# Performance work log

Measured on AMD Instinct MI355X. Metric: run time of the kernel, lower is better.

## Reference

```python
import jax, jax.numpy as jnp
import numpy as np

NUM_GROUPS = 32
EPS = 1e-6


def group_norm(x, gamma, beta):
    # x: [B, C, H, W]
    b, c, h, w = x.shape
    xg = x.reshape(b, NUM_GROUPS, c // NUM_GROUPS, h, w)
    mean = xg.mean(axis=(2, 3, 4), keepdims=True)
    var = xg.var(axis=(2, 3, 4), keepdims=True)
    xn = ((xg - mean) * jax.lax.rsqrt(var + EPS)).reshape(b, c, h, w)
    return xn * gamma[None, :, None, None] + beta[None, :, None, None]


def setup_inputs() -> dict:
    key = jax.random.key(0)
    ks = jax.random.split(key, 10)
    B, C, H, W = 2, 512, 64, 64
    s = 1.0 / np.sqrt(C)
    return {
        "x": jax.random.normal(ks[0], (B, C, H, W), dtype=jnp.float32),
        "gamma": jnp.ones((C,), jnp.float32),
        "beta": jnp.zeros((C,), jnp.float32),
        "Wq": jax.random.normal(ks[1], (C, C), jnp.float32) * s,
        "bq": jnp.zeros((C,), jnp.float32),
        "Wk": jax.random.normal(ks[2], (C, C), jnp.float32) * s,
        "bk": jnp.zeros((C,), jnp.float32),
        "Wv": jax.random.normal(ks[3], (C, C), jnp.float32) * s,
        "bv": jnp.zeros((C,), jnp.float32),
        "Wo": jax.random.normal(ks[4], (C, C), jnp.float32) * s,
        "bo": jnp.zeros((C,), jnp.float32),
    }


def reference(x, gamma, beta, Wq, bq, Wk, bk, Wv, bv, Wo, bo):
    b, c, h, w = x.shape
    hn = group_norm(x, gamma, beta)               # [B,C,H,W]
    hf = hn.reshape(b, c, h * w)                  # [B,C,N]
    # 1x1 convs == channel matmuls
    q = jnp.einsum('oc,bcn->bon', Wq, hf) + bq[None, :, None]
    k = jnp.einsum('oc,bcn->bon', Wk, hf) + bk[None, :, None]
    v = jnp.einsum('oc,bcn->bon', Wv, hf) + bv[None, :, None]
    scale = float(c) ** -0.5
    scores = jnp.einsum('bci,bcj->bij', q, k) * scale   # [B,N,N]
    attn = jax.nn.softmax(scores, axis=-1)
    out = jnp.einsum('bij,bcj->bci', attn, v)            # [B,C,N]
    out = jnp.einsum('oc,bcn->bon', Wo, out) + bo[None, :, None]
    return x + out.reshape(b, c, h, w)
```

## Files before the change

kernel.cpp:

```cpp
#include <hip/hip_runtime.h>

#define BB 2
#define CC 512
#define NS 4096
#define NGROUP 32
#define TILE 128
#define RSTRIDE 132

typedef __bf16 bf16_8 __attribute__((ext_vector_type(8)));
typedef __bf16 bf16_4 __attribute__((ext_vector_type(4)));
typedef float f32_4 __attribute__((ext_vector_type(4)));

#define SMEM_BYTES 33792

__device__ __forceinline__ void gld_lds16(const __bf16* g, __bf16* l) {
  __builtin_amdgcn_global_load_lds(
      (const __attribute__((address_space(1))) unsigned int*)g,
      (__attribute__((address_space(3))) unsigned int*)l, 16, 0, 0);
}

__global__ __launch_bounds__(256) void gn_stats(const float* __restrict__ x,
                                                float* __restrict__ stats) {
  const float4* p = (const float4*)(x + (size_t)blockIdx.x * 65536);
  float s = 0.f, q = 0.f;
  for (int i = threadIdx.x; i < 16384; i += 256) {
    float4 v = p[i];
    s += v.x + v.y + v.z + v.w;
    q += v.x * v.x + v.y * v.y + v.z * v.z + v.w * v.w;
  }
#pragma unroll
  for (int off = 32; off > 0; off >>= 1) {
    s += __shfl_down(s, off, 64);
    q += __shfl_down(q, off, 64);
  }
  __shared__ float ls[4], lq[4];
  int wave = threadIdx.x >> 6, lane = threadIdx.x & 63;
  if (lane == 0) { ls[wave] = s; lq[wave] = q; }
  __syncthreads();
  if (threadIdx.x == 0) {
    float S = ls[0] + ls[1] + ls[2] + ls[3];
    float Q = lq[0] + lq[1] + lq[2] + lq[3];
    float mean = S * (1.f / 65536.f);
    float var = Q * (1.f / 65536.f) - mean * mean;
    stats[blockIdx.x * 2] = mean;
    stats[blockIdx.x * 2 + 1] = rsqrtf(var + 1e-6f);
  }
}

__global__ __launch_bounds__(256) void gn_apply_t(const float* __restrict__ x,
                                                  const float* __restrict__ stats,
                                                  const float* __restrict__ gamma,
                                                  const float* __restrict__ beta,
                                                  __bf16* __restrict__ hnT) {
  __shared__ float tile[32][33];
  int b = blockIdx.z;
  int c0 = blockIdx.y * 32;
  int n0 = blockIdx.x * 32;
  int tx = threadIdx.x;
  int ty = threadIdx.y;
  const float* xb = x + (size_t)b * CC * NS;
#pragma unroll
  for (int i = 0; i < 4; i++) {
    int c = c0 + ty + i * 8;
    float mean = stats[(b * NGROUP + (c >> 4)) * 2 + 0];
    float rstd = stats[(b * NGROUP + (c >> 4)) * 2 + 1];
    float v = xb[(size_t)c * NS + n0 + tx];
    tile[ty + i * 8][tx] = (v - mean) * rstd * gamma[c] + beta[c];
  }
  __syncthreads();
  __bf16* out = hnT + (size_t)b * NS * CC;
#pragma unroll
  for (int i = 0; i < 4; i++) {
    int n = n0 + ty + i * 8;
    out[(size_t)n * CC + c0 + tx] = (__bf16)tile[tx][ty + i * 8];
  }
}

__global__ __launch_bounds__(256) void cvt_w(const float* __restrict__ w0, const float* __restrict__ w1,
                                             const float* __restrict__ w2, const float* __restrict__ w3,
                                             __bf16* __restrict__ o0, __bf16* __restrict__ o1,
                                             __bf16* __restrict__ o2, __bf16* __restrict__ o3) {
  int tsel = blockIdx.x >> 8;
  int i = (blockIdx.x & 255) * 256 + threadIdx.x;
  const float* src = tsel == 0 ? w0 : tsel == 1 ? w1 : tsel == 2 ? w2 : w3;
  __bf16* dst = tsel == 0 ? o0 : tsel == 1 ? o1 : tsel == 2 ? o2 : o3;
  float4 v = ((const float4*)src)[i];
  bf16_4 r;
  r[0] = (__bf16)v.x; r[1] = (__bf16)v.y; r[2] = (__bf16)v.z; r[3] = (__bf16)v.w;
  ((bf16_4*)dst)[i] = r;
}

__device__ __forceinline__ void gemm_core(const __bf16* __restrict__ A, const __bf16* __restrict__ B,
                                          int K, int lda, int ldb,
                                          __bf16* lA, __bf16* lB, f32_4 (&acc)[4][2]) {
  const int t = threadIdx.x;
  const int lane = t & 63;
  const int wave = t >> 6;
  const int lrow = lane & 15, quad = lane >> 4;
  const int wrow = (wave >> 2) * 64, wcol = (wave & 3) * 32;
  const int co = (quad ^ ((lrow >> 1) & 3)) * 8;
  const int r0 = t >> 2;
  const int kp = ((t & 3) ^ ((t >> 3) & 3)) * 8;
  const __bf16* pA = A + (size_t)r0 * lda + kp;
  const __bf16* pB = B + (size_t)r0 * ldb + kp;
  for (int k0 = 0; k0 < K; k0 += 64) {
    __syncthreads();
    gld_lds16(pA + k0,      &lA[t * 8]);
    gld_lds16(pA + k0 + 32, &lA[4096 + t * 8]);
    gld_lds16(pB + k0,      &lB[t * 8]);
    gld_lds16(pB + k0 + 32, &lB[4096 + t * 8]);
    __syncthreads();
#pragma unroll
    for (int ks = 0; ks < 2; ks++) {
      const __bf16* la = lA + ks * 4096;
      const __bf16* lb = lB + ks * 4096;
      bf16_8 af[4], bfr[2];
#pragma unroll
      for (int i = 0; i < 4; i++)
        af[i] = *(const bf16_8*)&la[(wrow + i * 16 + lrow) * 32 + co];
#pragma unroll
      for (int j = 0; j < 2; j++)
        bfr[j] = *(const bf16_8*)&lb[(wcol + j * 16 + lrow) * 32 + co];
#pragma unroll
      for (int i = 0; i < 4; i++)
#pragma unroll
        for (int j = 0; j < 2; j++)
          acc[i][j] = __builtin_amdgcn_mfma_f32_16x16x32_bf16(af[i], bfr[j], acc[i][j], 0, 0, 0);
    }
  }
}

__device__ __forceinline__ void stage_acc(float* ls, const f32_4 (&acc)[4][2], int pass) {
  const int t = threadIdx.x;
  const int lane = t & 63, wave = t >> 6;
  const int lrow = lane & 15, quad = lane >> 4;
  const int wrow = (wave >> 2) * 64, wcol = (wave & 3) * 32;
  if ((wrow >> 6) == pass) {
#pragma unroll
    for (int i = 0; i < 4; i++)
#pragma unroll
      for (int r = 0; r < 4; r++)
#pragma unroll
        for (int jj = 0; jj < 2; jj++)
          ls[(i * 16 + quad * 4 + r) * RSTRIDE + wcol + jj * 16 + lrow] = acc[i][jj][r];
  }
}

__device__ __forceinline__ void drain_bf16(const float* ls, __bf16* gdst, int ldg) {
  const int t = threadIdx.x;
#pragma unroll
  for (int k2 = 0; k2 < 4; k2++) {
    int idx = k2 * 512 + t;
    int row = idx >> 5, col = (idx & 31) * 4;
    f32_4 v = *(const f32_4*)&ls[row * RSTRIDE + col];
    bf16_4 o;
    o[0] = (__bf16)v[0]; o[1] = (__bf16)v[1]; o[2] = (__bf16)v[2]; o[3] = (__bf16)v[3];
    *(bf16_4*)&gdst[(size_t)row * ldg + col] = o;
  }
}

__device__ __forceinline__ void drain_f32(const float* ls, float* gdst, int ldg) {
  const int t = threadIdx.x;
#pragma unroll
  for (int k2 = 0; k2 < 4; k2++) {
    int idx = k2 * 512 + t;
    int row = idx >> 5, col = (idx & 31) * 4;
    f32_4 v = *(const f32_4*)&ls[row * RSTRIDE + col];
    float4 o = {v[0], v[1], v[2], v[3]};
    *(float4*)&gdst[(size_t)row * ldg + col] = o;
  }
}

__global__ __launch_bounds__(512, 4) void qkv_gemm(const __bf16* __restrict__ hnT,
                                                   const __bf16* __restrict__ Wq,
                                                   const __bf16* __restrict__ Wk,
                                                   const __bf16* __restrict__ Wv,
                                                   const float* __restrict__ bq,
                                                   const float* __restrict__ bk,
                                                   const float* __restrict__ bv,
                                                   __bf16* __restrict__ qT,
                                                   __bf16* __restrict__ kT,
                                                   __bf16* __restrict__ vv) {
  __shared__ char smem[SMEM_BYTES];
  __bf16* lA = (__bf16*)smem;
  __bf16* lB = (__bf16*)(smem + 16384);
  float* lsr = (float*)smem;
  const int b = blockIdx.z;
  const int id = blockIdx.x;
  const int sel = id >> 7;
  const int r = id & 127;
  const long long sBNC = (long long)NS * CC;
  const long long sBCN = (long long)CC * NS;

  int m0, n0, N;
  const __bf16 *Ap, *Bp;
  __bf16* Cp;
  const float* bias;
  if (sel < 2) {
    m0 = (r >> 2) * TILE;
    n0 = (r & 3) * TILE;
    Ap = hnT + (size_t)b * sBNC + (size_t)m0 * CC;
    Bp = (sel == 0 ? Wq : Wk) + (size_t)n0 * CC;
    Cp = (sel == 0 ? qT : kT) + (size_t)b * sBNC;
    bias = (sel == 0 ? bq : bk);
    N = CC;
  } else {
    m0 = (r & 3) * TILE;
    n0 = (r >> 2) * TILE;
    Ap = Wv + (size_t)m0 * CC;
    Bp = hnT + (size_t)b * sBNC + (size_t)n0 * CC;
    Cp = vv + (size_t)b * sBCN;
    bias = bv;
    N = NS;
  }

  f32_4 acc[4][2];
#pragma unroll
  for (int i = 0; i < 4; i++)
#pragma unroll
    for (int j = 0; j < 2; j++) acc[i][j] = {0.f, 0.f, 0.f, 0.f};

  gemm_core(Ap, Bp, CC, CC, CC, lA, lB, acc);

  const int t = threadIdx.x;
  const int lane = t & 63;
  const int lrow = lane & 15, quad = lane >> 4;
  const int wave = t >> 6;
  const int wrow = (wave >> 2) * 64, wcol = (wave & 3) * 32;
#pragma unroll
  for (int i = 0; i < 4; i++)
#pragma unroll
    for (int r2 = 0; r2 < 4; r2++) {
      float rowb = (sel == 2) ? bias[m0 + wrow + i * 16 + quad * 4 + r2] : 0.f;
#pragma unroll
      for (int j = 0; j < 2; j++) {
        float cb = (sel < 2) ? bias[n0 + wcol + j * 16 + lrow] : rowb;
        acc[i][j][r2] += cb;
      }
    }

#pragma unroll
  for (int p = 0; p < 2; p++) {
    __syncthreads();
    stage_acc(lsr, acc, p);
    __syncthreads();
    drain_bf16(lsr, Cp + (size_t)(m0 + p * 64) * N + n0, N);
  }
}

__global__ __launch_bounds__(512, 4) void e_gemm(const __bf16* __restrict__ qT,
                                                 const __bf16* __restrict__ kT,
                                                 __bf16* __restrict__ E,
                                                 float* __restrict__ l,
                                                 float scale) {
  __shared__ char smem[32768];
  __bf16* lA = (__bf16*)smem;
  __bf16* lB = (__bf16*)(smem + 16384);
  const int g = blockIdx.x;
  const int j = g & 7;
  const int b = j & 1;
  const int moct = j >> 1;
  const int k = g >> 3;
  const int sc = k >> 6;
  const int rem = k & 63;
  const int m0 = (moct * 8 + (rem >> 3)) * TILE;
  const int n0 = (sc * 8 + (rem & 7)) * TILE;
  const long long sBNC = (long long)NS * CC;
  const long long sBNN = (long long)NS * NS;
  const __bf16* Ap = qT + (size_t)b * sBNC + (size_t)m0 * CC;
  const __bf16* Bp = kT + (size_t)b * sBNC + (size_t)n0 * CC;

  f32_4 acc[4][2];
#pragma unroll
  for (int i = 0; i < 4; i++)
#pragma unroll
    for (int jj = 0; jj < 2; jj++) acc[i][jj] = {0.f, 0.f, 0.f, 0.f};

  gemm_core(Ap, Bp, CC, CC, CC, lA, lB, acc);

  const int t = threadIdx.x;
  const int lane = t & 63;
  const int lrow = lane & 15, quad = lane >> 4;
  const int wave = t >> 6;
  const int wrow = (wave >> 2) * 64, wcol = (wave & 3) * 32;
  __bf16* Ep = E + (size_t)b * sBNN;
  float* lp = l + (size_t)b * NS;
#pragma unroll
  for (int i = 0; i < 4; i++) {
#pragma unroll
    for (int r = 0; r < 4; r++) {
      int gm = m0 + wrow + i * 16 + quad * 4 + r;
      float rp = 0.f;
#pragma unroll
      for (int jj = 0; jj < 2; jj++) {
        int gn = n0 + wcol + jj * 16 + lrow;
        float ev = __expf(acc[i][jj][r] * scale);
        rp += ev;
        Ep[(size_t)gm * NS + gn] = (__bf16)ev;
      }
      rp += __shfl_down(rp, 8, 16);
      rp += __shfl_down(rp, 4, 16);
      rp += __shfl_down(rp, 2, 16);
      rp += __shfl_down(rp, 1, 16);
      if (lrow == 0) atomicAdd(&lp[gm], rp);
    }
  }
}

__global__ __launch_bounds__(512, 4) void ao_split4(const __bf16* __restrict__ E,
                                                    const __bf16* __restrict__ vv,
                                                    __bf16* __restrict__ p0,
                                                    __bf16* __restrict__ p1,
                                                    __bf16* __restrict__ p2,
                                                    __bf16* __restrict__ p3) {
  __shared__ char smem[SMEM_BYTES];
  __bf16* lA = (__bf16*)smem;
  __bf16* lB = (__bf16*)(smem + 16384);
  float* lsr = (float*)smem;
  const int g = blockIdx.x;
  const int j = g & 7;
  const int b = j & 1;
  const int split = j >> 1;
  const int k = g >> 3;
  const int m0 = (k >> 2) * TILE;
  const int n0 = (k & 3) * TILE;
  const long long sBNN = (long long)NS * NS;
  const long long sBCN = (long long)CC * NS;
  const long long sBNC = (long long)NS * CC;
  const __bf16* Ap = E + (size_t)b * sBNN + (size_t)m0 * NS + (size_t)split * 1024;
  const __bf16* Bp = vv + (size_t)b * sBCN + (size_t)n0 * NS + (size_t)split * 1024;
  __bf16* Cp = (split == 0 ? p0 : split == 1 ? p1 : split == 2 ? p2 : p3) + (size_t)b * sBNC;

  f32_4 acc[4][2];
#pragma unroll
  for (int i = 0; i < 4; i++)
#pragma unroll
    for (int jj = 0; jj < 2; jj++) acc[i][jj] = {0.f, 0.f, 0.f, 0.f};

  gemm_core(Ap, Bp, 1024, NS, NS, lA, lB, acc);

#pragma unroll
  for (int p = 0; p < 2; p++) {
    __syncthreads();
    stage_acc(lsr, acc, p);
    __syncthreads();
    drain_bf16(lsr, Cp + (size_t)(m0 + p * 64) * CC + n0, CC);
  }
}

__global__ __launch_bounds__(256) void reduce_ao4(const __bf16* __restrict__ p0,
                                                  const __bf16* __restrict__ p1,
                                                  const __bf16* __restrict__ p2,
                                                  const __bf16* __restrict__ p3,
                                                  const float* __restrict__ l,
                                                  __bf16* __restrict__ o) {
  int i = blockIdx.x * 256 + threadIdx.x;
  int row = i >> 6;
  float inv = 1.f / l[row];
  bf16_8 a = ((const bf16_8*)p0)[i];
  bf16_8 c = ((const bf16_8*)p1)[i];
  bf16_8 d = ((const bf16_8*)p2)[i];
  bf16_8 e = ((const bf16_8*)p3)[i];
  bf16_8 r;
#pragma unroll
  for (int k = 0; k < 8; k++)
    r[k] = (__bf16)(((float)a[k] + (float)c[k] + (float)d[k] + (float)e[k]) * inv);
  ((bf16_8*)o)[i] = r;
}

__global__ __launch_bounds__(512, 4) void wo_split(const __bf16* __restrict__ Wo,
                                                   const __bf16* __restrict__ aoT,
                                                   float* __restrict__ pw0,
                                                   float* __restrict__ pw1) {
  __shared__ char smem[SMEM_BYTES];
  __bf16* lA = (__bf16*)smem;
  __bf16* lB = (__bf16*)(smem + 16384);
  float* lsr = (float*)smem;
  const int b = blockIdx.z & 1;
  const int split = blockIdx.z >> 1;
  const int m0 = blockIdx.y * TILE;
  const int n0 = blockIdx.x * TILE;
  const long long sBNC = (long long)NS * CC;
  const long long sBCN = (long long)CC * NS;
  const __bf16* Ap = Wo + (size_t)m0 * CC + (size_t)split * 256;
  const __bf16* Bp = aoT + (size_t)b * sBNC + (size_t)n0 * CC + (size_t)split * 256;
  float* Cp = (split ? pw1 : pw0) + (size_t)b * sBCN;

  f32_4 acc[4][2];
#pragma unroll
  for (int i = 0; i < 4; i++)
#pragma unroll
    for (int j = 0; j < 2; j++) acc[i][j] = {0.f, 0.f, 0.f, 0.f};

  gemm_core(Ap, Bp, 256, CC, CC, lA, lB, acc);

#pragma unroll
  for (int p = 0; p < 2; p++) {
    __syncthreads();
    stage_acc(lsr, acc, p);
    __syncthreads();
    drain_f32(lsr, Cp + (size_t)(m0 + p * 64) * NS + n0, NS);
  }
}

__global__ __launch_bounds__(256) void final_out(const float* __restrict__ pw0,
                                                 const float* __restrict__ pw1,
                                                 const float* __restrict__ bo,
                                                 const float* __restrict__ x,
                                                 float* __restrict__ out) {
  int i = blockIdx.x * 256 + threadIdx.x;
  int o = (i >> 10) & (CC - 1);
  float bias = bo[o];
  float4 a = ((const float4*)pw0)[i];
  float4 c = ((const float4*)pw1)[i];
  float4 xr = ((const float4*)x)[i];
  float4 r;
  r.x = a.x + c.x + bias + xr.x;
  r.y = a.y + c.y + bias + xr.y;
  r.z = a.z + c.z + bias + xr.z;
  r.w = a.w + c.w + bias + xr.w;
  ((float4*)out)[i] = r;
}

extern "C" void kernel_launch(void* const* d_in, const int* in_sizes, int n_in,
                              void* d_out, int out_size, void* d_ws, size_t ws_size,
                              hipStream_t stream) {
  const float* x = (const float*)d_in[0];
  const float* gamma = (const float*)d_in[1];
  const float* beta = (const float*)d_in[2];
  const float* Wq = (const float*)d_in[3];
  const float* bq = (const float*)d_in[4];
  const float* Wk = (const float*)d_in[5];
  const float* bk = (const float*)d_in[6];
  const float* Wv = (const float*)d_in[7];
  const float* bv = (const float*)d_in[8];
  const float* Wo = (const float*)d_in[9];
  const float* bo = (const float*)d_in[10];
  float* out = (float*)d_out;

  char* ws = (char*)d_ws;
  __bf16* hnT = (__bf16*)(ws + 0);
  __bf16* qT  = (__bf16*)(ws + 8388608);
  __bf16* kT  = (__bf16*)(ws + 16777216);
  __bf16* vv  = (__bf16*)(ws + 25165824);
  __bf16* aoT = (__bf16*)(ws + 33554432);
  __bf16* Eb  = (__bf16*)(ws + 41943040);
  float* pw0  = (float*)(ws + 41943040);
  float* pw1  = (float*)(ws + 58720256);
  __bf16* Wqb = (__bf16*)(ws + 109051904);
  __bf16* Wkb = (__bf16*)(ws + 109576192);
  __bf16* Wvb = (__bf16*)(ws + 110100480);
  __bf16* Wob = (__bf16*)(ws + 110624768);
  float* stats = (float*)(ws + 111149056);
  float* lsum = (float*)(ws + 109051904);
  __bf16* p0 = hnT;
  __bf16* p1 = qT;
  __bf16* p2 = kT;
  __bf16* p3 = aoT;

  const float scale = 0.044194173824159216f;

  cvt_w<<<1024, 256, 0, stream>>>(Wq, Wk, Wv, Wo, Wqb, Wkb, Wvb, Wob);
  gn_stats<<<BB * NGROUP, 256, 0, stream>>>(x, stats);
  gn_apply_t<<<dim3(NS / 32, CC / 32, BB), dim3(32, 8), 0, stream>>>(x, stats, gamma, beta, hnT);

  qkv_gemm<<<dim3(384, 1, BB), 512, 0, stream>>>(hnT, Wqb, Wkb, Wvb, bq, bk, bv, qT, kT, vv);

  hipMemsetAsync(lsum, 0, BB * NS * sizeof(float), stream);
  e_gemm<<<2048, 512, 0, stream>>>(qT, kT, Eb, lsum, scale);

  ao_split4<<<1024, 512, 0, stream>>>(Eb, vv, p0, p1, p2, p3);
  reduce_ao4<<<2048, 256, 0, stream>>>(p0, p1, p2, p3, lsum, aoT);

  wo_split<<<dim3(NS / TILE, CC / TILE, 2 * BB), 512, 0, stream>>>(Wob, aoT, pw0, pw1);
  final_out<<<4096, 256, 0, stream>>>(pw0, pw1, bo, x, out);
}
```

Before: 252.2 us.

## Double K-step per barrier in GEMM core and store Wo partials as bf16

The shared GEMM core now loads a 128-wide K slab (four 32-wide planes) per pair of barriers instead of 64, which halves the synchronisation count and grows LDS per block to 64 KB. The Wo split-K partial sums are written as bf16 instead of fp32, halving the traffic into and out of the final residual-add kernel. The larger LDS footprint can lower occupancy below the 4 blocks per CU requested in the launch bounds, and the bf16 partials add rounding error to the output.

After: 270.9 us. 1.07x slower.

```diff
diff --git a/kernel.cpp b/kernel.cpp
--- a/kernel.cpp
+++ b/kernel.cpp
@@ -11,7 +11,7 @@
 typedef __bf16 bf16_4 __attribute__((ext_vector_type(4)));
 typedef float f32_4 __attribute__((ext_vector_type(4)));
 
-#define SMEM_BYTES 33792
+#define SMEM_BYTES 65536
 
 __device__ __forceinline__ void gld_lds16(const __bf16* g, __bf16* l) {
   __builtin_amdgcn_global_load_lds(
@@ -103,15 +103,16 @@
   const int kp = ((t & 3) ^ ((t >> 3) & 3)) * 8;
   const __bf16* pA = A + (size_t)r0 * lda + kp;
   const __bf16* pB = B + (size_t)r0 * ldb + kp;
-  for (int k0 = 0; k0 < K; k0 += 64) {
-    __syncthreads();
-    gld_lds16(pA + k0,      &lA[t * 8]);
-    gld_lds16(pA + k0 + 32, &lA[4096 + t * 8]);
-    gld_lds16(pB + k0,      &lB[t * 8]);
-    gld_lds16(pB + k0 + 32, &lB[4096 + t * 8]);
-    __syncthreads();
-#pragma unroll
-    for (int ks = 0; ks < 2; ks++) {
+  for (int k0 = 0; k0 < K; k0 += 128) {
+    __syncthreads();
+#pragma unroll
+    for (int pl = 0; pl < 4; pl++) {
+      gld_lds16(pA + k0 + pl * 32, &lA[pl * 4096 + t * 8]);
+      gld_lds16(pB + k0 + pl * 32, &lB[pl * 4096 + t * 8]);
+    }
+    __syncthreads();
+#pragma unroll
+    for (int ks = 0; ks < 4; ks++) {
       const __bf16* la = lA + ks * 4096;
       const __bf16* lb = lB + ks * 4096;
       bf16_8 af[4], bfr[2];
@@ -156,18 +157,6 @@
     bf16_4 o;
     o[0] = (__bf16)v[0]; o[1] = (__bf16)v[1]; o[2] = (__bf16)v[2]; o[3] = (__bf16)v[3];
     *(bf16_4*)&gdst[(size_t)row * ldg + col] = o;
-  }
-}
-
-__device__ __forceinline__ void drain_f32(const float* ls, float* gdst, int ldg) {
-  const int t = threadIdx.x;
-#pragma unroll
-  for (int k2 = 0; k2 < 4; k2++) {
-    int idx = k2 * 512 + t;
-    int row = idx >> 5, col = (idx & 31) * 4;
-    f32_4 v = *(const f32_4*)&ls[row * RSTRIDE + col];
-    float4 o = {v[0], v[1], v[2], v[3]};
-    *(float4*)&gdst[(size_t)row * ldg + col] = o;
   }
 }
 
@@ -183,7 +172,7 @@
                                                    __bf16* __restrict__ vv) {
   __shared__ char smem[SMEM_BYTES];
   __bf16* lA = (__bf16*)smem;
-  __bf16* lB = (__bf16*)(smem + 16384);
+  __bf16* lB = (__bf16*)(smem + 32768);
   float* lsr = (float*)smem;
   const int b = blockIdx.z;
   const int id = blockIdx.x;
@@ -253,9 +242,9 @@
                                                  __bf16* __restrict__ E,
                                                  float* __restrict__ l,
                                                  float scale) {
-  __shared__ char smem[32768];
+  __shared__ char smem[SMEM_BYTES];
   __bf16* lA = (__bf16*)smem;
-  __bf16* lB = (__bf16*)(smem + 16384);
+  __bf16* lB = (__bf16*)(smem + 32768);
   const int g = blockIdx.x;
   const int j = g & 7;
   const int b = j & 1;
@@ -315,7 +304,7 @@
                                                     __bf16* __restrict__ p3) {
   __shared__ char smem[SMEM_BYTES];
   __bf16* lA = (__bf16*)smem;
-  __bf16* lB = (__bf16*)(smem + 16384);
+  __bf16* lB = (__bf16*)(smem + 32768);
   float* lsr = (float*)smem;
   const int g = blockIdx.x;
   const int j = g & 7;
@@ -370,11 +359,11 @@
 
 __global__ __launch_bounds__(512, 4) void wo_split(const __bf16* __restrict__ Wo,
                                                    const __bf16* __restrict__ aoT,
-                                                   float* __restrict__ pw0,
-                                                   float* __restrict__ pw1) {
+                                                   __bf16* __restrict__ pw0,
+                                                   __bf16* __restrict__ pw1) {
   __shared__ char smem[SMEM_BYTES];
   __bf16* lA = (__bf16*)smem;
-  __bf16* lB = (__bf16*)(smem + 16384);
+  __bf16* lB = (__bf16*)(smem + 32768);
   float* lsr = (float*)smem;
   const int b = blockIdx.z & 1;
   const int split = blockIdx.z >> 1;
@@ -384,7 +373,7 @@
   const long long sBCN = (long long)CC * NS;
   const __bf16* Ap = Wo + (size_t)m0 * CC + (size_t)split * 256;
   const __bf16* Bp = aoT + (size_t)b * sBNC + (size_t)n0 * CC + (size_t)split * 256;
-  float* Cp = (split ? pw1 : pw0) + (size_t)b * sBCN;
+  __bf16* Cp = (split ? pw1 : pw0) + (size_t)b * sBCN;
 
   f32_4 acc[4][2];
 #pragma unroll
@@ -399,26 +388,26 @@
     __syncthreads();
     stage_acc(lsr, acc, p);
     __syncthreads();
-    drain_f32(lsr, Cp + (size_t)(m0 + p * 64) * NS + n0, NS);
-  }
-}
-
-__global__ __launch_bounds__(256) void final_out(const float* __restrict__ pw0,
-                                                 const float* __restrict__ pw1,
+    drain_bf16(lsr, Cp + (size_t)(m0 + p * 64) * NS + n0, NS);
+  }
+}
+
+__global__ __launch_bounds__(256) void final_out(const __bf16* __restrict__ pw0,
+                                                 const __bf16* __restrict__ pw1,
                                                  const float* __restrict__ bo,
                                                  const float* __restrict__ x,
                                                  float* __restrict__ out) {
   int i = blockIdx.x * 256 + threadIdx.x;
   int o = (i >> 10) & (CC - 1);
   float bias = bo[o];
-  float4 a = ((const float4*)pw0)[i];
-  float4 c = ((const float4*)pw1)[i];
+  bf16_4 a = ((const bf16_4*)pw0)[i];
+  bf16_4 c = ((const bf16_4*)pw1)[i];
   float4 xr = ((const float4*)x)[i];
   float4 r;
-  r.x = a.x + c.x + bias + xr.x;
-  r.y = a.y + c.y + bias + xr.y;
-  r.z = a.z + c.z + bias + xr.z;
-  r.w = a.w + c.w + bias + xr.w;
+  r.x = (float)a[0] + (float)c[0] + bias + xr.x;
+  r.y = (float)a[1] + (float)c[1] + bias + xr.y;
+  r.z = (float)a[2] + (float)c[2] + bias + xr.z;
+  r.w = (float)a[3] + (float)c[3] + bias + xr.w;
   ((float4*)out)[i] = r;
 }
 
@@ -445,8 +434,8 @@
   __bf16* vv  = (__bf16*)(ws + 25165824);
   __bf16* aoT = (__bf16*)(ws + 33554432);
   __bf16* Eb  = (__bf16*)(ws + 41943040);
-  float* pw0  = (float*)(ws + 41943040);
-  float* pw1  = (float*)(ws + 58720256);
+  __bf16* pw0 = (__bf16*)(ws + 41943040);
+  __bf16* pw1 = (__bf16*)(ws + 50331648);
   __bf16* Wqb = (__bf16*)(ws + 109051904);
   __bf16* Wkb = (__bf16*)(ws + 109576192);
   __bf16* Wvb = (__bf16*)(ws + 110100480);
```
